# Kernel optimization log

Measured on AMD Instinct MI355X. Metric: run time of the kernel, lower is better.

Reference implementation:

```python
import jax, jax.numpy as jnp
import numpy as np

WINDOW = 8  # window_size from init; keys per query = WINDOW + 1 (causal, inclusive of self)


def setup_inputs() -> dict:
    key = jax.random.key(0)
    ks = jax.random.split(key, 5)
    S, D, R = 32768, 1024, 256
    x = jax.random.normal(ks[0], (S, D), dtype=jnp.float32)
    Wq = jax.random.normal(ks[1], (D, R), dtype=jnp.float32) / D ** 0.5
    Wk = jax.random.normal(ks[2], (D, R), dtype=jnp.float32) / D ** 0.5
    Wv = jax.random.normal(ks[3], (D, R), dtype=jnp.float32) / D ** 0.5
    Wo = jax.random.normal(ks[4], (R, D), dtype=jnp.float32) / R ** 0.5
    bq = jnp.zeros((R,), dtype=jnp.float32)
    bk = jnp.zeros((R,), dtype=jnp.float32)
    bv = jnp.zeros((R,), dtype=jnp.float32)
    bo = jnp.zeros((D,), dtype=jnp.float32)
    return {"x": x, "Wq": Wq, "Wk": Wk, "Wv": Wv, "Wo": Wo,
            "bq": bq, "bk": bk, "bv": bv, "bo": bo}


def reference(x, Wq, Wk, Wv, Wo, bq, bk, bv, bo):
    S, D = x.shape
    R = Wq.shape[1]
    W = WINDOW + 1  # keys per query
    Q = x @ Wq + bq  # [S, R]
    K = x @ Wk + bk  # [S, R]
    V = x @ Wv + bv  # [S, R]
    # For query i, attend to positions i-WINDOW .. i (clamped at 0).
    offs = jnp.arange(-WINDOW, 1)                      # [W]
    idx = jnp.arange(S)[:, None] + offs[None, :]       # [S, W]
    valid = idx >= 0
    idxc = jnp.clip(idx, 0, S - 1)
    Kw = K[idxc]                                       # [S, W, R]
    Vw = V[idxc]                                       # [S, W, R]
    scores = jnp.einsum('sr,swr->sw', Q, Kw) / (R ** 0.5)
    scores = jnp.where(valid, scores, -jnp.inf)
    attn = jax.nn.softmax(scores, axis=-1)             # [S, W]
    ctx = jnp.einsum('sw,swr->sr', attn, Vw)           # [S, R]
    return ctx @ Wo + bo                               # [S, D]
```

## Files before the change

kernel.cpp:

```cpp
#include <hip/hip_runtime.h>
#include <stdint.h>


typedef __attribute__((ext_vector_type(8))) short short8;
typedef __attribute__((ext_vector_type(4))) float floatx4;

typedef __attribute__((address_space(1))) const void global_cv;
typedef __attribute__((address_space(3))) void lds_v;

__device__ __forceinline__ float b2f(unsigned short u) {
  union { float f; uint32_t i; } v; v.i = ((uint32_t)u) << 16; return v.f;
}
__device__ __forceinline__ unsigned short f2b(float f) {
  union { float f; uint32_t i; } v; v.f = f;
  uint32_t x = v.i;
  return (unsigned short)((x + 0x7FFFu + ((x >> 16) & 1u)) >> 16);
}
__device__ __forceinline__ uint32_t pack2bf(float a, float b) {
  uint32_t ua = (__float_as_uint(a) + 0x8000u) >> 16;
  uint32_t ub = (__float_as_uint(b) + 0x8000u) & 0xFFFF0000u;
  return ua | ub;
}

__device__ __forceinline__ void async16(const unsigned short* g, unsigned short* s) {
  __builtin_amdgcn_global_load_lds((global_cv*)g, (lds_v*)s, 16, 0, 0);
}

__device__ __forceinline__ void storeC(unsigned short* C, size_t idx, float v) {
  C[idx] = f2b(v);
}
__device__ __forceinline__ void storeC(float* C, size_t idx, float v) {
  C[idx] = v;
}

__global__ __launch_bounds__(256) void cvt_x(
    const float* __restrict__ x, unsigned short* __restrict__ xb, int n8)
{
  const int stride = gridDim.x * blockDim.x;
  for (int i = blockIdx.x * blockDim.x + threadIdx.x; i < n8; i += stride) {
    const float4 u = ((const float4*)x)[2 * i];
    const float4 v = ((const float4*)x)[2 * i + 1];
    uint4 pk;
    pk.x = pack2bf(u.x, u.y); pk.y = pack2bf(u.z, u.w);
    pk.z = pack2bf(v.x, v.y); pk.w = pack2bf(v.z, v.w);
    ((uint4*)xb)[i] = pk;
  }
}

template <typename CT, bool AF32, int NT>
__global__ __launch_bounds__(256) void gemm_bt(
    const void* __restrict__ Aptr,
    const unsigned short* __restrict__ Bt,
    const float* __restrict__ bias,
    CT* __restrict__ C,
    int K, int lda, int ldb, int ldc)
{
  __shared__ __align__(16) unsigned short sA[128 * 64];
  __shared__ __align__(16) unsigned short sB[128 * 64];

  const int tid = threadIdx.x;
  const int w   = tid >> 6;
  const int l   = tid & 63;
  const int l15 = l & 15;
  const int q   = l >> 4;

  const int bt  = blockIdx.x;
  const int xcd = bt & 7;
  const int j_  = bt >> 3;
  const int n0  = (j_ % NT) * 128;
  const int m0  = ((j_ / NT) * 8 + xcd) * 128;

  const int wm  = (w >> 1) * 64;
  const int wn  = (w & 1) * 64;

  floatx4 acc[4][4];
  #pragma unroll
  for (int i = 0; i < 4; ++i)
    #pragma unroll
    for (int j = 0; j < 4; ++j)
      #pragma unroll
      for (int t = 0; t < 4; ++t) acc[i][j][t] = 0.f;

  const int srow = l >> 3;
  const int sch  = l & 7;
  const int arow = tid >> 1;
  const int acb  = (tid & 1) * 4;

  for (int k0 = 0; k0 < K; k0 += 64) {
    #pragma unroll
    for (int jj = 0; jj < 4; ++jj) {
      const int rr = (jj * 4 + w) * 8 + srow;
      const int kc = sch ^ (rr & 7);
      async16(Bt + (size_t)(n0 + rr) * ldb + (k0 + kc * 8),
              sB + (jj * 4 + w) * 512);
    }
    if constexpr (AF32) {
      const float* A = (const float*)Aptr;
      const float* src = A + (size_t)(m0 + arow) * lda + k0 + acb * 8;
      #pragma unroll
      for (int c = 0; c < 4; ++c) {
        const float4 u = *(const float4*)(src + c * 8);
        const float4 v = *(const float4*)(src + c * 8 + 4);
        uint4 pk;
        pk.x = pack2bf(u.x, u.y); pk.y = pack2bf(u.z, u.w);
        pk.z = pack2bf(v.x, v.y); pk.w = pack2bf(v.z, v.w);
        const int pch = (acb + c) ^ (arow & 7);
        *(uint4*)(sA + arow * 64 + pch * 8) = pk;
      }
    } else {
      const unsigned short* A = (const unsigned short*)Aptr;
      #pragma unroll
      for (int jj = 0; jj < 4; ++jj) {
        const int rr = (jj * 4 + w) * 8 + srow;
        const int kc = sch ^ (rr & 7);
        async16(A + (size_t)(m0 + rr) * lda + (k0 + kc * 8),
                sA + (jj * 4 + w) * 512);
      }
    }
    __syncthreads();

    #pragma unroll
    for (int kt = 0; kt < 2; ++kt) {
      short8 af[4], bf[4];
      #pragma unroll
      for (int mt = 0; mt < 4; ++mt) {
        const int row = wm + mt * 16 + l15;
        const int pc  = (kt * 4 + q) ^ (row & 7);
        af[mt] = *(const short8*)(sA + row * 64 + pc * 8);
      }
      #pragma unroll
      for (int nt = 0; nt < 4; ++nt) {
        const int row = wn + nt * 16 + l15;
        const int pc  = (kt * 4 + q) ^ (row & 7);
        bf[nt] = *(const short8*)(sB + row * 64 + pc * 8);
      }
      #pragma unroll
      for (int mt = 0; mt < 4; ++mt)
        #pragma unroll
        for (int nt = 0; nt < 4; ++nt)
          acc[mt][nt] = __builtin_amdgcn_mfma_f32_16x16x32_bf16(
              af[mt], bf[nt], acc[mt][nt], 0, 0, 0);
    }
    __syncthreads();
  }

  #pragma unroll
  for (int nt = 0; nt < 4; ++nt) {
    const int col = n0 + wn + nt * 16 + l15;
    const float bs = bias[col];
    #pragma unroll
    for (int mt = 0; mt < 4; ++mt) {
      const int rbase = m0 + wm + mt * 16 + q * 4;
      #pragma unroll
      for (int r = 0; r < 4; ++r)
        storeC(C, (size_t)(rbase + r) * ldc + col, acc[mt][nt][r] + bs);
    }
  }
}

__global__ __launch_bounds__(256) void attn_win(unsigned short* QKV)
{
  const int l   = threadIdx.x & 63;
  const int grp = l >> 4;
  const int p   = l & 15;
  const int i   = blockIdx.x * 16 + (threadIdx.x >> 6) * 4 + grp;

  unsigned short* qrow = QKV + (size_t)i * 768 + p * 16;
  float qf[16];
  {
    const short8 v0 = *(const short8*)(qrow);
    const short8 v1 = *(const short8*)(qrow + 8);
    #pragma unroll
    for (int t = 0; t < 8; ++t) {
      qf[t]     = b2f((unsigned short)v0[t]);
      qf[8 + t] = b2f((unsigned short)v1[t]);
    }
  }

  float sc[9];
  #pragma unroll
  for (int wd = 0; wd < 9; ++wd) {
    const int j = i - 8 + wd;
    if (j >= 0) {
      const unsigned short* krow = QKV + (size_t)j * 768 + 256 + p * 16;
      const short8 v0 = *(const short8*)(krow);
      const short8 v1 = *(const short8*)(krow + 8);
      float d = 0.f;
      #pragma unroll
      for (int t = 0; t < 8; ++t) {
        d += qf[t]     * b2f((unsigned short)v0[t]);
        d += qf[8 + t] * b2f((unsigned short)v1[t]);
      }
      d += __shfl_xor(d, 8, 64);
      d += __shfl_xor(d, 4, 64);
      d += __shfl_xor(d, 2, 64);
      d += __shfl_xor(d, 1, 64);
      sc[wd] = d * 0.0625f;
    } else {
      sc[wd] = -1e30f;
    }
  }

  float mx = sc[0];
  #pragma unroll
  for (int wd = 1; wd < 9; ++wd) mx = fmaxf(mx, sc[wd]);
  float e[9], s = 0.f;
  #pragma unroll
  for (int wd = 0; wd < 9; ++wd) { e[wd] = __expf(sc[wd] - mx); s += e[wd]; }
  const float inv = 1.0f / s;

  float acc[16];
  #pragma unroll
  for (int t = 0; t < 16; ++t) acc[t] = 0.f;
  #pragma unroll
  for (int wd = 0; wd < 9; ++wd) {
    const int j = i - 8 + wd;
    if (j >= 0) {
      const unsigned short* vrow = QKV + (size_t)j * 768 + 512 + p * 16;
      const short8 v0 = *(const short8*)(vrow);
      const short8 v1 = *(const short8*)(vrow + 8);
      #pragma unroll
      for (int t = 0; t < 8; ++t) {
        acc[t]     += e[wd] * b2f((unsigned short)v0[t]);
        acc[8 + t] += e[wd] * b2f((unsigned short)v1[t]);
      }
    }
  }
  short8 o0, o1;
  #pragma unroll
  for (int t = 0; t < 8; ++t) {
    o0[t] = (short)f2b(acc[t] * inv);
    o1[t] = (short)f2b(acc[8 + t] * inv);
  }
  *(short8*)(qrow)     = o0;
  *(short8*)(qrow + 8) = o1;
}

__global__ __launch_bounds__(256) void prep_w(
    const float* __restrict__ Wq, const float* __restrict__ Wk,
    const float* __restrict__ Wv, const float* __restrict__ Wo,
    const float* __restrict__ bq, const float* __restrict__ bk,
    const float* __restrict__ bv, const float* __restrict__ bo,
    unsigned short* __restrict__ Wt,
    unsigned short* __restrict__ Wot,
    float* __restrict__ bias1,
    float* __restrict__ bias2)
{
  const int tt = blockIdx.x;
  if (tt < 1024) {
    __shared__ float tile[32][33];
    const float* src; unsigned short* dst; int N, Kd, k0, n0;
    if (tt < 768) {
      const int s = tt >> 8;
      const int r = tt & 255;
      src = (s == 0) ? Wq : (s == 1) ? Wk : Wv;
      N = 256; Kd = 1024;
      k0 = (r & 31) * 32;
      n0 = (r >> 5) * 32;
      dst = Wt + (size_t)s * 256 * 1024;
    } else {
      const int r = tt - 768;
      src = Wo; N = 1024; Kd = 256;
      k0 = (r & 7) * 32;
      n0 = (r >> 3) * 32;
      dst = Wot;
    }
    const int t  = threadIdx.x;
    const int rr = t >> 3;
    const int c4 = (t & 7) * 4;
    const float4 v = *(const float4*)(src + (size_t)(k0 + rr) * N + n0 + c4);
    tile[rr][c4 + 0] = v.x; tile[rr][c4 + 1] = v.y;
    tile[rr][c4 + 2] = v.z; tile[rr][c4 + 3] = v.w;
    __syncthreads();
    ushort4 o;
    o.x = f2b(tile[c4 + 0][rr]); o.y = f2b(tile[c4 + 1][rr]);
    o.z = f2b(tile[c4 + 2][rr]); o.w = f2b(tile[c4 + 3][rr]);
    *(ushort4*)(dst + (size_t)(n0 + rr) * Kd + k0 + c4) = o;
  } else {
    for (int c = threadIdx.x; c < 1792; c += 256) {
      if (c < 768)
        bias1[c] = (c < 256) ? bq[c] : (c < 512) ? bk[c - 256] : bv[c - 512];
      else
        bias2[c - 768] = bo[c - 768];
    }
  }
}

extern "C" void kernel_launch(void* const* d_in, const int* in_sizes, int n_in,
                              void* d_out, int out_size, void* d_ws, size_t ws_size,
                              hipStream_t stream) {
  const float* x  = (const float*)d_in[0];
  const float* Wq = (const float*)d_in[1];
  const float* Wk = (const float*)d_in[2];
  const float* Wv = (const float*)d_in[3];
  const float* Wo = (const float*)d_in[4];
  const float* bq = (const float*)d_in[5];
  const float* bk = (const float*)d_in[6];
  const float* bv = (const float*)d_in[7];
  const float* bo = (const float*)d_in[8];
  float* out = (float*)d_out;

  unsigned short* ws    = (unsigned short*)d_ws;
  unsigned short* Wt    = ws;
  unsigned short* Wot   = Wt  + 786432;
  float*          bias1 = (float*)(Wot + 262144);
  float*          bias2 = bias1 + 768;
  unsigned short* QKV   = (unsigned short*)(bias2 + 1024);
  unsigned short* xb;
  const size_t need = 119544832;
  if (ws_size >= need) xb = QKV + 25165824;
  else                 xb = (unsigned short*)d_out;

  prep_w<<<1025, 256, 0, stream>>>(Wq, Wk, Wv, Wo, bq, bk, bv, bo,
                                   Wt, Wot, bias1, bias2);

  cvt_x<<<2048, 256, 0, stream>>>(x, xb, 32768 * 1024 / 8);

  gemm_bt<unsigned short, false, 6><<<1536, 256, 0, stream>>>(
      (const void*)xb, Wt, bias1, QKV, 1024, 1024, 1024, 768);

  attn_win<<<2048, 256, 0, stream>>>(QKV);

  gemm_bt<float, false, 8><<<2048, 256, 0, stream>>>(
      (const void*)QKV, Wot, bias2, out, 256, 768, 256, 1024);
}
```

Measured before the change: 363.0 us.

## Replace GEMM with 256x256-tile, 8-wave, triple-buffered pipelined kernel

Both projection GEMMs move from a 128x128 tile with 4 waves and single-buffered LDS to a 256x256 tile with 8 waves. The new kernel triple-buffers K=32 slices, issuing async global-to-LDS loads ahead of use and ordering them with explicit vmcnt waits and raw barriers. It also raises wave priority around the MFMA blocks. The aim is to overlap memory loads with matrix math and raise data reuse per tile, at the cost of higher register and LDS pressure and fewer, larger blocks.

```diff
diff --git a/kernel.cpp b/kernel.cpp
--- a/kernel.cpp
+++ b/kernel.cpp
@@ -47,16 +47,16 @@
   }
 }
 
-template <typename CT, bool AF32, int NT>
-__global__ __launch_bounds__(256) void gemm_bt(
-    const void* __restrict__ Aptr,
+template <typename CT, int NTB>
+__global__ __launch_bounds__(512, 2) void gemm8(
+    const unsigned short* __restrict__ A,
     const unsigned short* __restrict__ Bt,
     const float* __restrict__ bias,
     CT* __restrict__ C,
     int K, int lda, int ldb, int ldc)
 {
-  __shared__ __align__(16) unsigned short sA[128 * 64];
-  __shared__ __align__(16) unsigned short sB[128 * 64];
+  __shared__ __align__(16) unsigned short sA[3][256 * 32];
+  __shared__ __align__(16) unsigned short sB[3][256 * 32];
 
   const int tid = threadIdx.x;
   const int w   = tid >> 6;
@@ -64,96 +64,114 @@
   const int l15 = l & 15;
   const int q   = l >> 4;
 
+  const int wm  = (w >> 2) * 128;
+  const int wn  = (w & 3) * 64;
+
   const int bt  = blockIdx.x;
   const int xcd = bt & 7;
   const int j_  = bt >> 3;
-  const int n0  = (j_ % NT) * 128;
-  const int m0  = ((j_ / NT) * 8 + xcd) * 128;
-
-  const int wm  = (w >> 1) * 64;
-  const int wn  = (w & 1) * 64;
-
-  floatx4 acc[4][4];
-  #pragma unroll
-  for (int i = 0; i < 4; ++i)
+  const int n0  = (j_ % NTB) * 256;
+  const int m0  = ((j_ / NTB) * 8 + xcd) * 256;
+
+  const int sr  = l >> 2;
+  const int pcs = l & 3;
+  const int lc  = pcs ^ ((sr >> 1) & 3);
+  const unsigned short* Ap[2];
+  const unsigned short* Bp[2];
+  #pragma unroll
+  for (int j = 0; j < 2; ++j) {
+    const int rr = j * 128 + w * 16 + sr;
+    Ap[j] = A  + (size_t)(m0 + rr) * lda + lc * 8;
+    Bp[j] = Bt + (size_t)(n0 + rr) * ldb + lc * 8;
+  }
+
+  floatx4 acc[8][4];
+  #pragma unroll
+  for (int i = 0; i < 8; ++i)
     #pragma unroll
     for (int j = 0; j < 4; ++j)
       #pragma unroll
       for (int t = 0; t < 4; ++t) acc[i][j][t] = 0.f;
 
-  const int srow = l >> 3;
-  const int sch  = l & 7;
-  const int arow = tid >> 1;
-  const int acb  = (tid & 1) * 4;
-
-  for (int k0 = 0; k0 < K; k0 += 64) {
-    #pragma unroll
-    for (int jj = 0; jj < 4; ++jj) {
-      const int rr = (jj * 4 + w) * 8 + srow;
-      const int kc = sch ^ (rr & 7);
-      async16(Bt + (size_t)(n0 + rr) * ldb + (k0 + kc * 8),
-              sB + (jj * 4 + w) * 512);
-    }
-    if constexpr (AF32) {
-      const float* A = (const float*)Aptr;
-      const float* src = A + (size_t)(m0 + arow) * lda + k0 + acb * 8;
-      #pragma unroll
-      for (int c = 0; c < 4; ++c) {
-        const float4 u = *(const float4*)(src + c * 8);
-        const float4 v = *(const float4*)(src + c * 8 + 4);
-        uint4 pk;
-        pk.x = pack2bf(u.x, u.y); pk.y = pack2bf(u.z, u.w);
-        pk.z = pack2bf(v.x, v.y); pk.w = pack2bf(v.z, v.w);
-        const int pch = (acb + c) ^ (arow & 7);
-        *(uint4*)(sA + arow * 64 + pch * 8) = pk;
-      }
+  const int fpc  = (q ^ ((l15 >> 1) & 3)) * 8;
+  const int arow = (wm + l15) * 32 + fpc;
+  const int brow = (wn + l15) * 32 + fpc;
+
+  const int NT = K >> 5;
+
+  #pragma unroll
+  for (int j = 0; j < 2; ++j) async16(Ap[j],      sA[0] + (j * 128 + w * 16) * 32);
+  #pragma unroll
+  for (int j = 0; j < 2; ++j) async16(Bp[j],      sB[0] + (j * 128 + w * 16) * 32);
+  #pragma unroll
+  for (int j = 0; j < 2; ++j) async16(Ap[j] + 32, sA[1] + (j * 128 + w * 16) * 32);
+  #pragma unroll
+  for (int j = 0; j < 2; ++j) async16(Bp[j] + 32, sB[1] + (j * 128 + w * 16) * 32);
+  asm volatile("s_waitcnt vmcnt(4)" ::: "memory");
+  __builtin_amdgcn_s_barrier();
+
+  int bc = 0, bs = 2, k2 = 64;
+  for (int t = 0; t < NT; ++t) {
+    short8 bf[4], af[4];
+    #pragma unroll
+    for (int nt = 0; nt < 4; ++nt)
+      bf[nt] = *(const short8*)(sB[bc] + brow + nt * 512);
+    #pragma unroll
+    for (int mt = 0; mt < 4; ++mt)
+      af[mt] = *(const short8*)(sA[bc] + arow + mt * 512);
+    if (k2 < K) {
+      #pragma unroll
+      for (int j = 0; j < 2; ++j)
+        async16(Ap[j] + k2, sA[bs] + (j * 128 + w * 16) * 32);
+    }
+    __builtin_amdgcn_s_barrier();
+    __builtin_amdgcn_s_setprio(1);
+    #pragma unroll
+    for (int mt = 0; mt < 4; ++mt)
+      #pragma unroll
+      for (int nt = 0; nt < 4; ++nt)
+        acc[mt][nt] = __builtin_amdgcn_mfma_f32_16x16x32_bf16(
+            af[mt], bf[nt], acc[mt][nt], 0, 0, 0);
+    __builtin_amdgcn_s_setprio(0);
+    __builtin_amdgcn_s_barrier();
+
+    #pragma unroll
+    for (int mt = 0; mt < 4; ++mt)
+      af[mt] = *(const short8*)(sA[bc] + arow + (mt + 4) * 512);
+    if (k2 < K) {
+      #pragma unroll
+      for (int j = 0; j < 2; ++j)
+        async16(Bp[j] + k2, sB[bs] + (j * 128 + w * 16) * 32);
+      asm volatile("s_waitcnt vmcnt(4)" ::: "memory");
     } else {
-      const unsigned short* A = (const unsigned short*)Aptr;
-      #pragma unroll
-      for (int jj = 0; jj < 4; ++jj) {
-        const int rr = (jj * 4 + w) * 8 + srow;
-        const int kc = sch ^ (rr & 7);
-        async16(A + (size_t)(m0 + rr) * lda + (k0 + kc * 8),
-                sA + (jj * 4 + w) * 512);
-      }
-    }
-    __syncthreads();
-
-    #pragma unroll
-    for (int kt = 0; kt < 2; ++kt) {
-      short8 af[4], bf[4];
-      #pragma unroll
-      for (int mt = 0; mt < 4; ++mt) {
-        const int row = wm + mt * 16 + l15;
-        const int pc  = (kt * 4 + q) ^ (row & 7);
-        af[mt] = *(const short8*)(sA + row * 64 + pc * 8);
-      }
-      #pragma unroll
-      for (int nt = 0; nt < 4; ++nt) {
-        const int row = wn + nt * 16 + l15;
-        const int pc  = (kt * 4 + q) ^ (row & 7);
-        bf[nt] = *(const short8*)(sB + row * 64 + pc * 8);
-      }
-      #pragma unroll
-      for (int mt = 0; mt < 4; ++mt)
-        #pragma unroll
-        for (int nt = 0; nt < 4; ++nt)
-          acc[mt][nt] = __builtin_amdgcn_mfma_f32_16x16x32_bf16(
-              af[mt], bf[nt], acc[mt][nt], 0, 0, 0);
-    }
-    __syncthreads();
+      asm volatile("s_waitcnt vmcnt(0)" ::: "memory");
+    }
+    __builtin_amdgcn_s_barrier();
+    __builtin_amdgcn_s_setprio(1);
+    #pragma unroll
+    for (int mt = 0; mt < 4; ++mt)
+      #pragma unroll
+      for (int nt = 0; nt < 4; ++nt)
+        acc[4 + mt][nt] = __builtin_amdgcn_mfma_f32_16x16x32_bf16(
+            af[mt], bf[nt], acc[4 + mt][nt], 0, 0, 0);
+    __builtin_amdgcn_s_setprio(0);
+    __builtin_amdgcn_s_barrier();
+
+    bc = (bc == 2) ? 0 : bc + 1;
+    bs = (bs == 2) ? 0 : bs + 1;
+    k2 += 32;
   }
 
   #pragma unroll
   for (int nt = 0; nt < 4; ++nt) {
     const int col = n0 + wn + nt * 16 + l15;
-    const float bs = bias[col];
-    #pragma unroll
-    for (int mt = 0; mt < 4; ++mt) {
+    const float bsv = bias[col];
+    #pragma unroll
+    for (int mt = 0; mt < 8; ++mt) {
       const int rbase = m0 + wm + mt * 16 + q * 4;
       #pragma unroll
       for (int r = 0; r < 4; ++r)
-        storeC(C, (size_t)(rbase + r) * ldc + col, acc[mt][nt][r] + bs);
+        storeC(C, (size_t)(rbase + r) * ldc + col, acc[mt][nt][r] + bsv);
     }
   }
 }
@@ -316,11 +334,11 @@
 
   cvt_x<<<2048, 256, 0, stream>>>(x, xb, 32768 * 1024 / 8);
 
-  gemm_bt<unsigned short, false, 6><<<1536, 256, 0, stream>>>(
-      (const void*)xb, Wt, bias1, QKV, 1024, 1024, 1024, 768);
+  gemm8<unsigned short, 3><<<384, 512, 0, stream>>>(
+      xb, Wt, bias1, QKV, 1024, 1024, 1024, 768);
 
   attn_win<<<2048, 256, 0, stream>>>(QKV);
 
-  gemm_bt<float, false, 8><<<2048, 256, 0, stream>>>(
-      (const void*)QKV, Wot, bias2, out, 256, 768, 256, 1024);
-}
+  gemm8<float, 4><<<512, 512, 0, stream>>>(
+      QKV, Wot, bias2, out, 256, 768, 256, 1024);
+}
```

New measurement: 389.9 us. +7.4%, slower.

## Triple-buffer GEMM LDS tiles with async prefetch two stages ahead

Applied to the files above, without the earlier changes.

Rewrites the GEMM main loop to use BK=32 tiles in a three-stage LDS ring buffer, issuing async global-to-LDS loads two k-steps ahead and waiting on vmcnt instead of a full sync pair per iteration. It also drops the unused fp32-A conversion path and changes the LDS swizzle to fit the narrower tile. The goal is to overlap global memory latency with MFMA work, at the cost of more loop iterations and a single barrier per step.

```diff
diff --git a/kernel.cpp b/kernel.cpp
--- a/kernel.cpp
+++ b/kernel.cpp
@@ -47,16 +47,16 @@
   }
 }
 
-template <typename CT, bool AF32, int NT>
+template <typename CT, int NTB>
 __global__ __launch_bounds__(256) void gemm_bt(
-    const void* __restrict__ Aptr,
+    const unsigned short* __restrict__ A,
     const unsigned short* __restrict__ Bt,
     const float* __restrict__ bias,
     CT* __restrict__ C,
     int K, int lda, int ldb, int ldc)
 {
-  __shared__ __align__(16) unsigned short sA[128 * 64];
-  __shared__ __align__(16) unsigned short sB[128 * 64];
+  __shared__ __align__(16) unsigned short sA[3][128 * 32];
+  __shared__ __align__(16) unsigned short sB[3][128 * 32];
 
   const int tid = threadIdx.x;
   const int w   = tid >> 6;
@@ -67,8 +67,8 @@
   const int bt  = blockIdx.x;
   const int xcd = bt & 7;
   const int j_  = bt >> 3;
-  const int n0  = (j_ % NT) * 128;
-  const int m0  = ((j_ / NT) * 8 + xcd) * 128;
+  const int n0  = (j_ % NTB) * 128;
+  const int m0  = ((j_ / NTB) * 8 + xcd) * 128;
 
   const int wm  = (w >> 1) * 64;
   const int wn  = (w & 1) * 64;
@@ -81,68 +81,68 @@
       #pragma unroll
       for (int t = 0; t < 4; ++t) acc[i][j][t] = 0.f;
 
-  const int srow = l >> 3;
-  const int sch  = l & 7;
-  const int arow = tid >> 1;
-  const int acb  = (tid & 1) * 4;
-
-  for (int k0 = 0; k0 < K; k0 += 64) {
-    #pragma unroll
-    for (int jj = 0; jj < 4; ++jj) {
-      const int rr = (jj * 4 + w) * 8 + srow;
-      const int kc = sch ^ (rr & 7);
-      async16(Bt + (size_t)(n0 + rr) * ldb + (k0 + kc * 8),
-              sB + (jj * 4 + w) * 512);
-    }
-    if constexpr (AF32) {
-      const float* A = (const float*)Aptr;
-      const float* src = A + (size_t)(m0 + arow) * lda + k0 + acb * 8;
-      #pragma unroll
-      for (int c = 0; c < 4; ++c) {
-        const float4 u = *(const float4*)(src + c * 8);
-        const float4 v = *(const float4*)(src + c * 8 + 4);
-        uint4 pk;
-        pk.x = pack2bf(u.x, u.y); pk.y = pack2bf(u.z, u.w);
-        pk.z = pack2bf(v.x, v.y); pk.w = pack2bf(v.z, v.w);
-        const int pch = (acb + c) ^ (arow & 7);
-        *(uint4*)(sA + arow * 64 + pch * 8) = pk;
-      }
+  const int sr  = l >> 2;
+  const int pc_ = l & 3;
+  const int lc  = pc_ ^ ((sr >> 1) & 3);
+  const unsigned short* Asrc[2];
+  const unsigned short* Bsrc[2];
+  #pragma unroll
+  for (int j = 0; j < 2; ++j) {
+    const int rr = (w * 2 + j) * 16 + sr;
+    Asrc[j] = A  + (size_t)(m0 + rr) * lda + lc * 8;
+    Bsrc[j] = Bt + (size_t)(n0 + rr) * ldb + lc * 8;
+  }
+
+  const int fq   = (q ^ ((l15 >> 1) & 3)) * 8;
+  const int aoff = (wm + l15) * 32 + fq;
+  const int boff = (wn + l15) * 32 + fq;
+
+  const int KT = K >> 5;
+
+  #define STAGE(k0, b)                                                   \
+    {                                                                    \
+      _Pragma("unroll")                                                  \
+      for (int j = 0; j < 2; ++j) {                                      \
+        async16(Asrc[j] + (k0), &sA[b][(w * 2 + j) * 512]);              \
+        async16(Bsrc[j] + (k0), &sB[b][(w * 2 + j) * 512]);              \
+      }                                                                  \
+    }
+
+  STAGE(0, 0);
+  STAGE(32, 1);
+  asm volatile("s_waitcnt vmcnt(4)" ::: "memory");
+  __builtin_amdgcn_s_barrier();
+
+  int bc = 0;
+  for (int t = 0; t < KT; ++t) {
+    const int k2 = (t + 2) << 5;
+    const int bs = (bc == 0) ? 2 : bc - 1;
+    if (k2 < K) STAGE(k2, bs);
+
+    short8 af[4], bf[4];
+    #pragma unroll
+    for (int mt = 0; mt < 4; ++mt)
+      af[mt] = *(const short8*)(&sA[bc][aoff + mt * 512]);
+    #pragma unroll
+    for (int nt = 0; nt < 4; ++nt)
+      bf[nt] = *(const short8*)(&sB[bc][boff + nt * 512]);
+
+    #pragma unroll
+    for (int mt = 0; mt < 4; ++mt)
+      #pragma unroll
+      for (int nt = 0; nt < 4; ++nt)
+        acc[mt][nt] = __builtin_amdgcn_mfma_f32_16x16x32_bf16(
+            af[mt], bf[nt], acc[mt][nt], 0, 0, 0);
+
+    if (k2 < K) {
+      asm volatile("s_waitcnt vmcnt(4)" ::: "memory");
     } else {
-      const unsigned short* A = (const unsigned short*)Aptr;
-      #pragma unroll
-      for (int jj = 0; jj < 4; ++jj) {
-        const int rr = (jj * 4 + w) * 8 + srow;
-        const int kc = sch ^ (rr & 7);
-        async16(A + (size_t)(m0 + rr) * lda + (k0 + kc * 8),
-                sA + (jj * 4 + w) * 512);
-      }
-    }
-    __syncthreads();
-
-    #pragma unroll
-    for (int kt = 0; kt < 2; ++kt) {
-      short8 af[4], bf[4];
-      #pragma unroll
-      for (int mt = 0; mt < 4; ++mt) {
-        const int row = wm + mt * 16 + l15;
-        const int pc  = (kt * 4 + q) ^ (row & 7);
-        af[mt] = *(const short8*)(sA + row * 64 + pc * 8);
-      }
-      #pragma unroll
-      for (int nt = 0; nt < 4; ++nt) {
-        const int row = wn + nt * 16 + l15;
-        const int pc  = (kt * 4 + q) ^ (row & 7);
-        bf[nt] = *(const short8*)(sB + row * 64 + pc * 8);
-      }
-      #pragma unroll
-      for (int mt = 0; mt < 4; ++mt)
-        #pragma unroll
-        for (int nt = 0; nt < 4; ++nt)
-          acc[mt][nt] = __builtin_amdgcn_mfma_f32_16x16x32_bf16(
-              af[mt], bf[nt], acc[mt][nt], 0, 0, 0);
-    }
-    __syncthreads();
-  }
+      asm volatile("s_waitcnt vmcnt(0)" ::: "memory");
+    }
+    if (t + 1 < KT) __builtin_amdgcn_s_barrier();
+    bc = (bc == 2) ? 0 : bc + 1;
+  }
+  #undef STAGE
 
   #pragma unroll
   for (int nt = 0; nt < 4; ++nt) {
@@ -316,11 +316,11 @@
 
   cvt_x<<<2048, 256, 0, stream>>>(x, xb, 32768 * 1024 / 8);
 
-  gemm_bt<unsigned short, false, 6><<<1536, 256, 0, stream>>>(
-      (const void*)xb, Wt, bias1, QKV, 1024, 1024, 1024, 768);
+  gemm_bt<unsigned short, 6><<<1536, 256, 0, stream>>>(
+      xb, Wt, bias1, QKV, 1024, 1024, 1024, 768);
 
   attn_win<<<2048, 256, 0, stream>>>(QKV);
 
-  gemm_bt<float, false, 8><<<2048, 256, 0, stream>>>(
-      (const void*)QKV, Wot, bias2, out, 256, 768, 256, 1024);
-}
+  gemm_bt<float, 8><<<2048, 256, 0, stream>>>(
+      QKV, Wot, bias2, out, 256, 768, 256, 1024);
+}
```

New measurement: 364.2 us. About the same (+0.3%).
